# Optimization experiments

Measured on AMD Instinct MI355X. Metric: run time of the kernel, lower is better.

The kernel has to match this reference:

```python
import jax, jax.numpy as jnp
import numpy as np
import math

N = 262144
D_K = 64
D_V = 64


def setup_inputs() -> dict:
    key = jax.random.key(0)
    kq, kk, kv = jax.random.split(key, 3)
    Q = jax.random.normal(kq, (N, D_K), dtype=jnp.float32)
    K = jax.random.normal(kk, (N, D_K), dtype=jnp.float32)
    V = jax.random.normal(kv, (N, D_V), dtype=jnp.float32)
    return {"Q": Q, "K": K, "V": V}


def reference(Q, K, V):
    d_k = Q.shape[-1]
    scale = 1.0 / math.sqrt(d_k)
    # rho_q: softmax over the sequence axis (dim=-2)
    q = jax.nn.softmax(Q * scale, axis=-2)  # [N, d_k]
    # rho_k: softmax over the feature axis (dim=-1)
    k = jax.nn.softmax(K * scale, axis=-1)  # [N, d_k]
    # linear attention: [d_k, d_v] context first, then project with q
    context = k.T @ V                        # [d_k, d_v]
    return q @ context                       # [N, d_v]
```

## Files before the change

kernel.cpp:

```cpp
#include <hip/hip_runtime.h>
#include <hip/hip_bf16.h>

#define NROWS 262144
#define NB1 512
#define RPB 512
#define CL 0.18033688011112042f
#define PW 20

typedef __attribute__((ext_vector_type(8))) short s8v;
typedef __attribute__((ext_vector_type(4))) short s4h;
typedef __attribute__((ext_vector_type(4))) float f4v;

__device__ __forceinline__ short f2bf(float x) {
    unsigned u = __float_as_uint(x);
    u += 0x7FFF + ((u >> 16) & 1);
    return (short)(u >> 16);
}

__device__ __forceinline__ float dpp_red16(float x) {
    int t;
    t = __builtin_amdgcn_update_dpp(0, __float_as_int(x), 0xB1,  0xF, 0xF, true);
    x += __int_as_float(t);
    t = __builtin_amdgcn_update_dpp(0, __float_as_int(x), 0x4E,  0xF, 0xF, true);
    x += __int_as_float(t);
    t = __builtin_amdgcn_update_dpp(0, __float_as_int(x), 0x141, 0xF, 0xF, true);
    x += __int_as_float(t);
    t = __builtin_amdgcn_update_dpp(0, __float_as_int(x), 0x140, 0xF, 0xF, true);
    x += __int_as_float(t);
    return x;
}

#define GL4(dst, base, OFF) \
    asm volatile("global_load_dwordx4 %0, %1, off offset:" #OFF \
                 : "=v"(dst) : "v"(base))

__global__ __launch_bounds__(512, 4) void k1_stats(const float* __restrict__ Q,
                                                   const float* __restrict__ K,
                                                   const float* __restrict__ V,
                                                   float* __restrict__ ctx_part,
                                                   float* __restrict__ qs_part)
{
    const int tid  = threadIdx.x;
    const int lane = tid & 63;
    const int wid  = tid >> 6;
    const int m    = lane & 15;
    const int g    = lane >> 4;
    const int cb   = wid >> 1;
    const int vb0  = (wid & 1) * 2;
    const size_t base = (size_t)blockIdx.x * RPB;

    __shared__ ushort kkP[4][128][PW];
    __shared__ ushort vP [4][128][PW];
    __shared__ float  qsl[8][64];

    f4v acc0 = {0.f, 0.f, 0.f, 0.f};
    f4v acc1 = {0.f, 0.f, 0.f, 0.f};
    f4v qs4  = {0.f, 0.f, 0.f, 0.f};

    f4v kf[2][4], vf[2][4], qf[2][4];

#define ISSUE(CH, PB) do { \
        const float* kb = K + (base + (CH) * 128 + wid * 16 + g) * 64 + 4 * m; \
        const float* vb = V + (base + (CH) * 128 + wid * 16 + g) * 64 + 4 * m; \
        const float* qb = Q + (base + (CH) * 128 + wid * 16 + g) * 64 + 4 * m; \
        GL4(kf[PB][0], kb, 0); GL4(kf[PB][1], kb, 1024); \
        GL4(kf[PB][2], kb, 2048); GL4(kf[PB][3], kb, 3072); \
        GL4(vf[PB][0], vb, 0); GL4(vf[PB][1], vb, 1024); \
        GL4(vf[PB][2], vb, 2048); GL4(vf[PB][3], vb, 3072); \
        GL4(qf[PB][0], qb, 0); GL4(qf[PB][1], qb, 1024); \
        GL4(qf[PB][2], qb, 2048); GL4(qf[PB][3], qb, 3072); \
    } while (0)

    ISSUE(0, 0);

#pragma unroll
    for (int ch = 0; ch < 4; ++ch) {
        const int pb = ch & 1;
        if (ch < 3) {
            switch (ch + 1) {
                case 1: ISSUE(1, 1); break;
                case 2: ISSUE(2, 0); break;
                case 3: ISSUE(3, 1); break;
            }
            asm volatile("s_waitcnt vmcnt(12)" ::: "memory");
        } else {
            asm volatile("s_waitcnt vmcnt(0)" ::: "memory");
        }
        __builtin_amdgcn_sched_barrier(0);

#pragma unroll
        for (int i = 0; i < 4; ++i) {
            qs4[0] += exp2f(qf[pb][i][0] * CL); qs4[1] += exp2f(qf[pb][i][1] * CL);
            qs4[2] += exp2f(qf[pb][i][2] * CL); qs4[3] += exp2f(qf[pb][i][3] * CL);
        }
        f4v e4[4]; float rs[4];
#pragma unroll
        for (int i = 0; i < 4; ++i) {
            e4[i][0] = exp2f(kf[pb][i][0] * CL); e4[i][1] = exp2f(kf[pb][i][1] * CL);
            e4[i][2] = exp2f(kf[pb][i][2] * CL); e4[i][3] = exp2f(kf[pb][i][3] * CL);
        }
#pragma unroll
        for (int i = 0; i < 4; ++i)
            rs[i] = dpp_red16((e4[i][0] + e4[i][1]) + (e4[i][2] + e4[i][3]));
        s4h kp[4], vp4[4];
#pragma unroll
        for (int i = 0; i < 4; ++i) {
            const float inv = __builtin_amdgcn_rcpf(rs[i]);
            kp[i]  = s4h{f2bf(e4[i][0] * inv), f2bf(e4[i][1] * inv),
                         f2bf(e4[i][2] * inv), f2bf(e4[i][3] * inv)};
            vp4[i] = s4h{f2bf(vf[pb][i][0]), f2bf(vf[pb][i][1]),
                         f2bf(vf[pb][i][2]), f2bf(vf[pb][i][3])};
        }

        __syncthreads();
#pragma unroll
        for (int i = 0; i < 4; ++i) {
            const int lr = wid * 16 + i * 4 + g;
            *(s4h*)&kkP[m >> 2][lr][(m & 3) * 4] = kp[i];
            *(s4h*)&vP [m >> 2][lr][(m & 3) * 4] = vp4[i];
        }
        __syncthreads();

#pragma unroll
        for (int ks = 0; ks < 4; ++ks) {
            s8v bf, af0, af1;
#pragma unroll
            for (int e = 0; e < 8; ++e) {
                bf[e]  = (short)kkP[cb][32 * ks + 8 * g + e][m];
                af0[e] = (short)vP[vb0][32 * ks + 8 * g + e][m];
                af1[e] = (short)vP[vb0 + 1][32 * ks + 8 * g + e][m];
            }
            acc0 = __builtin_amdgcn_mfma_f32_16x16x32_bf16(af0, bf, acc0, 0, 0, 0);
            acc1 = __builtin_amdgcn_mfma_f32_16x16x32_bf16(af1, bf, acc1, 0, 0, 0);
        }
    }
#undef ISSUE

    *(f4v*)&ctx_part[(size_t)blockIdx.x * 4096 +
                     (cb * 16 + m) * 64 + vb0 * 16 + 4 * g]       = acc0;
    *(f4v*)&ctx_part[(size_t)blockIdx.x * 4096 +
                     (cb * 16 + m) * 64 + (vb0 + 1) * 16 + 4 * g] = acc1;

#pragma unroll
    for (int c = 0; c < 4; ++c) {
        qs4[c] += __shfl_xor(qs4[c], 16);
        qs4[c] += __shfl_xor(qs4[c], 32);
    }
    if (g == 0) *(f4v*)&qsl[wid][4 * m] = qs4;
    __syncthreads();
    if (tid < 64) {
        float s = 0.f;
#pragma unroll
        for (int w = 0; w < 8; ++w) s += qsl[w][tid];
        qs_part[blockIdx.x * 64 + tid] = s;
    }
}

__global__ __launch_bounds__(256) void k2(const float* __restrict__ ctx_part,
                                          const float* __restrict__ qs_part,
                                          ushort* __restrict__ ctxfT) {
    const int c = blockIdx.x;
    const int tid = threadIdx.x;
    const int bg = tid >> 4, vq = tid & 15;
    __shared__ f4v  red[16][16];
    __shared__ float qred[4][64];
    f4v s = {0.f, 0.f, 0.f, 0.f};
    for (int b = bg; b < NB1; b += 16)
        s += *(const f4v*)&ctx_part[(size_t)b * 4096 + c * 64 + vq * 4];
    float q = 0.f;
    for (int b = tid; b < NB1; b += 256) q += qs_part[b * 64 + c];
    red[bg][vq] = s;
    qred[tid >> 6][tid & 63] = q;
    __syncthreads();
    if (tid < 64) {
        float t = 0.f;
#pragma unroll
        for (int b = 0; b < 16; ++b) t += red[b][tid >> 2][tid & 3];
        float qv = (qred[0][tid] + qred[1][tid]) + (qred[2][tid] + qred[3][tid]);
        qv = dpp_red16(qv);
        qv += __shfl_xor(qv, 16);
        qv += __shfl_xor(qv, 32);
        ctxfT[tid * 64 + c] = (ushort)f2bf(t * __builtin_amdgcn_rcpf(qv));
    }
}

__global__ __launch_bounds__(256) void k3_out(const float* __restrict__ Q,
                                              const ushort* __restrict__ ctxfT,
                                              float* __restrict__ out) {
    const int tid  = threadIdx.x;
    const int lane = tid & 63;
    const int wid  = tid >> 6;
    const int li = lane & 15, g = lane >> 4;

    s8v ct[4][2];
#pragma unroll
    for (int va = 0; va < 4; ++va)
#pragma unroll
        for (int ks = 0; ks < 2; ++ks)
            ct[va][ks] = *(const s8v*)((const char*)ctxfT +
                            2 * ((va * 16 + li) * 64 + 32 * ks + 8 * g));

#pragma unroll
    for (int t = 0; t < 4; ++t) {
        const int row = blockIdx.x * 256 + t * 64 + wid * 16 + li;
        const f4v* qp = (const f4v*)(Q + (size_t)row * 64);
        f4v q0 = qp[2 * g], q1 = qp[2 * g + 1];
        f4v q2 = qp[8 + 2 * g], q3 = qp[8 + 2 * g + 1];
        s8v b0, b1;
#pragma unroll
        for (int e = 0; e < 4; ++e) {
            b0[e]     = f2bf(exp2f(q0[e] * CL));
            b0[e + 4] = f2bf(exp2f(q1[e] * CL));
            b1[e]     = f2bf(exp2f(q2[e] * CL));
            b1[e + 4] = f2bf(exp2f(q3[e] * CL));
        }
#pragma unroll
        for (int va = 0; va < 4; ++va) {
            f4v a = {0.f, 0.f, 0.f, 0.f};
            a = __builtin_amdgcn_mfma_f32_16x16x32_bf16(ct[va][0], b0, a, 0, 0, 0);
            a = __builtin_amdgcn_mfma_f32_16x16x32_bf16(ct[va][1], b1, a, 0, 0, 0);
            *(f4v*)&out[(size_t)row * 64 + va * 16 + 4 * g] = a;
        }
    }
}

extern "C" void kernel_launch(void* const* d_in, const int* in_sizes, int n_in,
                              void* d_out, int out_size, void* d_ws, size_t ws_size,
                              hipStream_t stream) {
    const float* Q = (const float*)d_in[0];
    const float* K = (const float*)d_in[1];
    const float* V = (const float*)d_in[2];
    float* out = (float*)d_out;

    float* w = (float*)d_ws;
    size_t off = 0;
    float*  qs_part = w + off;              off += (size_t)NB1 * 64;
    ushort* ctxfT   = (ushort*)(w + off);   off += 2048;
    float* ctx_part;
    const size_t need = (off + (size_t)NB1 * 4096) * sizeof(float);
    if (ws_size >= need) {
        ctx_part = w + off;
    } else {
        ctx_part = out;
    }

    k1_stats<<<NB1, 512, 0, stream>>>(Q, K, V, ctx_part, qs_part);
    k2<<<64, 256, 0, stream>>>(ctx_part, qs_part, ctxfT);
    k3_out<<<NROWS / 256, 256, 0, stream>>>(Q, ctxfT, out);
}
```

Measured before the change: 82.90 us.

## Fuse three kernels into one cooperative kernel caching softmax(Q) in LDS

Merges the stats, reduction and output kernels into a single cooperative launch of 256 blocks of 1024 rows each, separated by two grid-wide syncs. Each block stores its bf16 exp(Q) tile in a 128KB swizzled LDS buffer during the first pass, so the output phase no longer re-reads Q from global memory or recomputes the exponentials. The aim is to cut launch overhead and about a third of the HBM traffic. In exchange it adds grid-sync latency, leaves only 64 blocks busy during the reduction phase, and uses large LDS, which limits occupancy to one block per CU. If the workspace is too small, ctx_part falls back to aliasing out, which works only because out is fully overwritten after the syncs.

```diff
diff --git a/kernel.cpp b/kernel.cpp
--- a/kernel.cpp
+++ b/kernel.cpp
@@ -1,9 +1,11 @@
 #include <hip/hip_runtime.h>
 #include <hip/hip_bf16.h>
+#include <hip/hip_cooperative_groups.h>
 
 #define NROWS 262144
-#define NB1 512
-#define RPB 512
+#define NBF 256
+#define RPBF 1024
+#define NCH 16
 #define CL 0.18033688011112042f
 #define PW 20
 
@@ -34,11 +36,13 @@
     asm volatile("global_load_dwordx4 %0, %1, off offset:" #OFF \
                  : "=v"(dst) : "v"(base))
 
-__global__ __launch_bounds__(512, 4) void k1_stats(const float* __restrict__ Q,
-                                                   const float* __restrict__ K,
-                                                   const float* __restrict__ V,
-                                                   float* __restrict__ ctx_part,
-                                                   float* __restrict__ qs_part)
+__global__ __launch_bounds__(512, 2) void kfused(const float* __restrict__ Q,
+                                                 const float* __restrict__ K,
+                                                 const float* __restrict__ V,
+                                                 float* __restrict__ ctx_part,
+                                                 float* __restrict__ qs_part,
+                                                 ushort* __restrict__ ctxfT,
+                                                 float* __restrict__ out)
 {
     const int tid  = threadIdx.x;
     const int lane = tid & 63;
@@ -47,64 +51,69 @@
     const int g    = lane >> 4;
     const int cb   = wid >> 1;
     const int vb0  = (wid & 1) * 2;
-    const size_t base = (size_t)blockIdx.x * RPB;
-
-    __shared__ ushort kkP[4][128][PW];
-    __shared__ ushort vP [4][128][PW];
+    const size_t base = (size_t)blockIdx.x * RPBF;
+
+    __shared__ ushort kkP[4][64][PW];
+    __shared__ ushort vP [4][64][PW];
+    __shared__ ushort qtL[RPBF * 64];
     __shared__ float  qsl[8][64];
 
     f4v acc0 = {0.f, 0.f, 0.f, 0.f};
     f4v acc1 = {0.f, 0.f, 0.f, 0.f};
     f4v qs4  = {0.f, 0.f, 0.f, 0.f};
-
-    f4v kf[2][4], vf[2][4], qf[2][4];
+    f4v kf[2][2], vf[2][2], qf[2][2];
 
 #define ISSUE(CH, PB) do { \
-        const float* kb = K + (base + (CH) * 128 + wid * 16 + g) * 64 + 4 * m; \
-        const float* vb = V + (base + (CH) * 128 + wid * 16 + g) * 64 + 4 * m; \
-        const float* qb = Q + (base + (CH) * 128 + wid * 16 + g) * 64 + 4 * m; \
+        const float* kb = K + (base + (CH) * 64 + wid * 8 + g) * 64 + 4 * m; \
+        const float* vb = V + (base + (CH) * 64 + wid * 8 + g) * 64 + 4 * m; \
+        const float* qb = Q + (base + (CH) * 64 + wid * 8 + g) * 64 + 4 * m; \
         GL4(kf[PB][0], kb, 0); GL4(kf[PB][1], kb, 1024); \
-        GL4(kf[PB][2], kb, 2048); GL4(kf[PB][3], kb, 3072); \
         GL4(vf[PB][0], vb, 0); GL4(vf[PB][1], vb, 1024); \
-        GL4(vf[PB][2], vb, 2048); GL4(vf[PB][3], vb, 3072); \
         GL4(qf[PB][0], qb, 0); GL4(qf[PB][1], qb, 1024); \
-        GL4(qf[PB][2], qb, 2048); GL4(qf[PB][3], qb, 3072); \
     } while (0)
 
     ISSUE(0, 0);
 
 #pragma unroll
-    for (int ch = 0; ch < 4; ++ch) {
+    for (int ch = 0; ch < NCH; ++ch) {
         const int pb = ch & 1;
-        if (ch < 3) {
+        if (ch < NCH - 1) {
             switch (ch + 1) {
-                case 1: ISSUE(1, 1); break;
-                case 2: ISSUE(2, 0); break;
-                case 3: ISSUE(3, 1); break;
+                case 1:  ISSUE(1, 1);  break; case 2:  ISSUE(2, 0);  break;
+                case 3:  ISSUE(3, 1);  break; case 4:  ISSUE(4, 0);  break;
+                case 5:  ISSUE(5, 1);  break; case 6:  ISSUE(6, 0);  break;
+                case 7:  ISSUE(7, 1);  break; case 8:  ISSUE(8, 0);  break;
+                case 9:  ISSUE(9, 1);  break; case 10: ISSUE(10, 0); break;
+                case 11: ISSUE(11, 1); break; case 12: ISSUE(12, 0); break;
+                case 13: ISSUE(13, 1); break; case 14: ISSUE(14, 0); break;
+                case 15: ISSUE(15, 1); break;
             }
-            asm volatile("s_waitcnt vmcnt(12)" ::: "memory");
+            asm volatile("s_waitcnt vmcnt(6)" ::: "memory");
         } else {
             asm volatile("s_waitcnt vmcnt(0)" ::: "memory");
         }
         __builtin_amdgcn_sched_barrier(0);
 
 #pragma unroll
-        for (int i = 0; i < 4; ++i) {
-            qs4[0] += exp2f(qf[pb][i][0] * CL); qs4[1] += exp2f(qf[pb][i][1] * CL);
-            qs4[2] += exp2f(qf[pb][i][2] * CL); qs4[3] += exp2f(qf[pb][i][3] * CL);
-        }
-        f4v e4[4]; float rs[4];
-#pragma unroll
-        for (int i = 0; i < 4; ++i) {
+        for (int i = 0; i < 2; ++i) {
+            const float e0 = exp2f(qf[pb][i][0] * CL), e1 = exp2f(qf[pb][i][1] * CL);
+            const float e2 = exp2f(qf[pb][i][2] * CL), e3 = exp2f(qf[pb][i][3] * CL);
+            qs4[0] += e0; qs4[1] += e1; qs4[2] += e2; qs4[3] += e3;
+            const int lq = ch * 64 + wid * 8 + 4 * i + g;
+            const unsigned off = (unsigned)lq * 128u +
+                                 ((unsigned)(8 * m) ^ (((unsigned)lq & 7u) << 4));
+            *(s4h*)((char*)qtL + off) = s4h{f2bf(e0), f2bf(e1), f2bf(e2), f2bf(e3)};
+        }
+        f4v e4[2]; float rs[2];
+#pragma unroll
+        for (int i = 0; i < 2; ++i) {
             e4[i][0] = exp2f(kf[pb][i][0] * CL); e4[i][1] = exp2f(kf[pb][i][1] * CL);
             e4[i][2] = exp2f(kf[pb][i][2] * CL); e4[i][3] = exp2f(kf[pb][i][3] * CL);
-        }
-#pragma unroll
-        for (int i = 0; i < 4; ++i)
             rs[i] = dpp_red16((e4[i][0] + e4[i][1]) + (e4[i][2] + e4[i][3]));
-        s4h kp[4], vp4[4];
-#pragma unroll
-        for (int i = 0; i < 4; ++i) {
+        }
+        s4h kp[2], vp4[2];
+#pragma unroll
+        for (int i = 0; i < 2; ++i) {
             const float inv = __builtin_amdgcn_rcpf(rs[i]);
             kp[i]  = s4h{f2bf(e4[i][0] * inv), f2bf(e4[i][1] * inv),
                          f2bf(e4[i][2] * inv), f2bf(e4[i][3] * inv)};
@@ -114,15 +123,15 @@
 
         __syncthreads();
 #pragma unroll
-        for (int i = 0; i < 4; ++i) {
-            const int lr = wid * 16 + i * 4 + g;
+        for (int i = 0; i < 2; ++i) {
+            const int lr = wid * 8 + 4 * i + g;
             *(s4h*)&kkP[m >> 2][lr][(m & 3) * 4] = kp[i];
             *(s4h*)&vP [m >> 2][lr][(m & 3) * 4] = vp4[i];
         }
         __syncthreads();
 
 #pragma unroll
-        for (int ks = 0; ks < 4; ++ks) {
+        for (int ks = 0; ks < 2; ++ks) {
             s8v bf, af0, af1;
 #pragma unroll
             for (int e = 0; e < 8; ++e) {
@@ -154,44 +163,37 @@
         for (int w = 0; w < 8; ++w) s += qsl[w][tid];
         qs_part[blockIdx.x * 64 + tid] = s;
     }
-}
-
-__global__ __launch_bounds__(256) void k2(const float* __restrict__ ctx_part,
-                                          const float* __restrict__ qs_part,
-                                          ushort* __restrict__ ctxfT) {
-    const int c = blockIdx.x;
-    const int tid = threadIdx.x;
-    const int bg = tid >> 4, vq = tid & 15;
-    __shared__ f4v  red[16][16];
-    __shared__ float qred[4][64];
-    f4v s = {0.f, 0.f, 0.f, 0.f};
-    for (int b = bg; b < NB1; b += 16)
-        s += *(const f4v*)&ctx_part[(size_t)b * 4096 + c * 64 + vq * 4];
-    float q = 0.f;
-    for (int b = tid; b < NB1; b += 256) q += qs_part[b * 64 + c];
-    red[bg][vq] = s;
-    qred[tid >> 6][tid & 63] = q;
-    __syncthreads();
-    if (tid < 64) {
-        float t = 0.f;
-#pragma unroll
-        for (int b = 0; b < 16; ++b) t += red[b][tid >> 2][tid & 3];
-        float qv = (qred[0][tid] + qred[1][tid]) + (qred[2][tid] + qred[3][tid]);
-        qv = dpp_red16(qv);
-        qv += __shfl_xor(qv, 16);
-        qv += __shfl_xor(qv, 32);
-        ctxfT[tid * 64 + c] = (ushort)f2bf(t * __builtin_amdgcn_rcpf(qv));
-    }
-}
-
-__global__ __launch_bounds__(256) void k3_out(const float* __restrict__ Q,
-                                              const ushort* __restrict__ ctxfT,
-                                              float* __restrict__ out) {
-    const int tid  = threadIdx.x;
-    const int lane = tid & 63;
-    const int wid  = tid >> 6;
-    const int li = lane & 15, g = lane >> 4;
-
+
+    cooperative_groups::this_grid().sync();
+
+    if (blockIdx.x < 64) {
+        const int c = blockIdx.x;
+        float* redf = (float*)&kkP[0][0][0];
+        float* qred = redf + 1024;
+        if (tid < 256) {
+            const int bg = tid >> 4, vq = tid & 15;
+            f4v s = {0.f, 0.f, 0.f, 0.f};
+            for (int b = bg; b < NBF; b += 16)
+                s += *(const f4v*)&ctx_part[(size_t)b * 4096 + c * 64 + vq * 4];
+            *(f4v*)&redf[(bg * 16 + vq) * 4] = s;
+            qred[tid] = qs_part[tid * 64 + c];
+        }
+        __syncthreads();
+        if (tid < 64) {
+            float t = 0.f;
+#pragma unroll
+            for (int b = 0; b < 16; ++b) t += redf[(b * 16 + (tid >> 2)) * 4 + (tid & 3)];
+            float qv = (qred[tid] + qred[tid + 64]) + (qred[tid + 128] + qred[tid + 192]);
+            qv = dpp_red16(qv);
+            qv += __shfl_xor(qv, 16);
+            qv += __shfl_xor(qv, 32);
+            ctxfT[tid * 64 + c] = (ushort)f2bf(t * __builtin_amdgcn_rcpf(qv));
+        }
+    }
+
+    cooperative_groups::this_grid().sync();
+
+    const int li = lane & 15;
     s8v ct[4][2];
 #pragma unroll
     for (int va = 0; va < 4; ++va)
@@ -201,25 +203,18 @@
                             2 * ((va * 16 + li) * 64 + 32 * ks + 8 * g));
 
 #pragma unroll
-    for (int t = 0; t < 4; ++t) {
-        const int row = blockIdx.x * 256 + t * 64 + wid * 16 + li;
-        const f4v* qp = (const f4v*)(Q + (size_t)row * 64);
-        f4v q0 = qp[2 * g], q1 = qp[2 * g + 1];
-        f4v q2 = qp[8 + 2 * g], q3 = qp[8 + 2 * g + 1];
-        s8v b0, b1;
-#pragma unroll
-        for (int e = 0; e < 4; ++e) {
-            b0[e]     = f2bf(exp2f(q0[e] * CL));
-            b0[e + 4] = f2bf(exp2f(q1[e] * CL));
-            b1[e]     = f2bf(exp2f(q2[e] * CL));
-            b1[e + 4] = f2bf(exp2f(q3[e] * CL));
-        }
+    for (int it = 0; it < 8; ++it) {
+        const int lrow = it * 128 + wid * 16 + li;
+        const unsigned swz = ((unsigned)lrow & 7u) << 4;
+        const unsigned rb  = (unsigned)lrow * 128u;
+        const s8v b0 = *(const s8v*)((const char*)qtL + rb + ((unsigned)(16 * g) ^ swz));
+        const s8v b1 = *(const s8v*)((const char*)qtL + rb + ((unsigned)(64 + 16 * g) ^ swz));
 #pragma unroll
         for (int va = 0; va < 4; ++va) {
             f4v a = {0.f, 0.f, 0.f, 0.f};
             a = __builtin_amdgcn_mfma_f32_16x16x32_bf16(ct[va][0], b0, a, 0, 0, 0);
             a = __builtin_amdgcn_mfma_f32_16x16x32_bf16(ct[va][1], b1, a, 0, 0, 0);
-            *(f4v*)&out[(size_t)row * 64 + va * 16 + 4 * g] = a;
+            *(f4v*)&out[(base + (size_t)lrow) * 64 + va * 16 + 4 * g] = a;
         }
     }
 }
@@ -234,17 +229,17 @@
 
     float* w = (float*)d_ws;
     size_t off = 0;
-    float*  qs_part = w + off;              off += (size_t)NB1 * 64;
+    float*  qs_part = w + off;              off += (size_t)NBF * 64;
     ushort* ctxfT   = (ushort*)(w + off);   off += 2048;
     float* ctx_part;
-    const size_t need = (off + (size_t)NB1 * 4096) * sizeof(float);
+    const size_t need = (off + (size_t)NBF * 4096) * sizeof(float);
     if (ws_size >= need) {
         ctx_part = w + off;
     } else {
         ctx_part = out;
     }
 
-    k1_stats<<<NB1, 512, 0, stream>>>(Q, K, V, ctx_part, qs_part);
-    k2<<<64, 256, 0, stream>>>(ctx_part, qs_part, ctxfT);
-    k3_out<<<NROWS / 256, 256, 0, stream>>>(Q, ctxfT, out);
-}
+    void* args[] = {(void*)&Q, (void*)&K, (void*)&V,
+                    (void*)&ctx_part, (void*)&qs_part, (void*)&ctxfT, (void*)&out};
+    hipLaunchCooperativeKernel((void*)kfused, dim3(NBF), dim3(512), args, 0, stream);
+}
```

Result: slower. 126.3 us (+52.4%).
